# Optimization experiments

Measured on AMD Instinct MI355X. Metric: run time of the kernel, lower is better.

## Reference

```python
import jax, jax.numpy as jnp
import numpy as np

B, S, D, H, M, V, R = 2, 1024, 768, 8, 3072, 32000, 2
HD = D // H  # head_dim = qkv_dim // num_heads


def ln(x, scale, bias, eps=1e-6):
    m = jnp.mean(x, axis=-1, keepdims=True)
    v = jnp.mean(jnp.square(x - m), axis=-1, keepdims=True)
    return (x - m) * jax.lax.rsqrt(v + eps) * scale + bias


def setup_inputs() -> dict:
    key = jax.random.key(0)
    ks = jax.random.split(key, 16)
    r = lambda i, shp, s=0.02: jax.random.normal(ks[i], shp, jnp.float32) * s
    z = lambda shp: jnp.zeros(shp, jnp.float32)
    o = lambda shp: jnp.ones(shp, jnp.float32)
    return {
        'l2r_embed': jax.random.normal(ks[0], (B, S, D), jnp.float32),
        'r2l_embed': jax.random.normal(ks[1], (B, S, D), jnp.float32),
        'temb': jax.random.normal(ks[2], (B, D), jnp.float32),
        'ln_l2r_s': o((D,)), 'ln_l2r_b': z((D,)),
        'ln_r2l_s': o((D,)), 'ln_r2l_b': z((D,)),
        'Wq': r(3, (D, H, HD)), 'bq': z((H, HD)),
        'Wk': r(4, (D, H, HD)), 'bk': z((H, HD)),
        'Wv': r(5, (D, H, HD)), 'bv': z((H, HD)),
        'Wo': r(6, (H, HD, D)), 'bo': z((D,)),
        'ff_ln_s': o((D,)), 'ff_ln_b': z((D,)),
        'ff_w1': r(7, (D, M)), 'ff_b1': z((M,)),
        'ff_w2': r(8, (M, D)), 'ff_b2': z((D,)),
        'tm_w1': r(9, (D, M)), 'tm_b1': z((M,)),
        'tm_w2': r(10, (M, 4 * D)), 'tm_b2': z((4 * D,)),
        'film_w': r(11, (R, 4 * D, 2 * D)), 'film_b': z((R, 2 * D)),
        'r_w1': r(12, (R, D, M)), 'r_b1': z((R, M)),
        'r_w2': r(13, (R, M, D)), 'r_b2': z((R, D)),
        'r_ln_s': o((R, D)), 'r_ln_b': z((R, D)),
        'out_w': r(14, (D, V)), 'out_b': z((V,)),
    }


def reference(l2r_embed, r2l_embed, temb, ln_l2r_s, ln_l2r_b, ln_r2l_s, ln_r2l_b,
              Wq, bq, Wk, bk, Wv, bv, Wo, bo, ff_ln_s, ff_ln_b,
              ff_w1, ff_b1, ff_w2, ff_b2, tm_w1, tm_b1, tm_w2, tm_b2,
              film_w, film_b, r_w1, r_b1, r_w2, r_b2, r_ln_s, r_ln_b,
              out_w, out_b):
    inputs = l2r_embed + r2l_embed
    # prenorm on each direction (temb stays raw)
    l2r_n = ln(l2r_embed, ln_l2r_s, ln_l2r_b)
    r2l_n = ln(r2l_embed, ln_r2l_s, ln_r2l_b)
    # cross attention: query from sum, keys/vals from [temb, l2r, r2l]
    q = jnp.einsum('bsd,dhk->bshk', l2r_n + r2l_n, Wq) + bq
    all_e = jnp.concatenate([temb[:, None, :], l2r_n, r2l_n], axis=1)  # [B, 2S+1, D]
    k = jnp.einsum('bsd,dhk->bshk', all_e, Wk) + bk
    v = jnp.einsum('bsd,dhk->bshk', all_e, Wv) + bv
    q = q / jnp.sqrt(jnp.float32(HD))
    logits = jnp.einsum('bqhd,bkhd->bhqk', q, k)  # [B, H, S, 2S+1]
    idx = jnp.arange(S)
    l2r_mask = idx[:, None] >= idx[None, :]
    r2l_mask = idx[:, None] <= idx[None, :]
    joint = jnp.concatenate(
        [jnp.ones((S, 1), bool), l2r_mask, r2l_mask], axis=-1)[None, None]
    aw = jax.nn.softmax(
        jnp.where(joint, logits, jnp.finfo(jnp.float32).min), axis=-1)
    x = jnp.einsum('bhqk,bkhd->bqhd', aw, v)
    x = jnp.einsum('bqhd,hde->bqe', x, Wo) + bo
    x = x + inputs
    # prenorm FF block
    z = ln(x, ff_ln_s, ff_ln_b)
    z = jax.nn.relu(z @ ff_w1 + ff_b1) @ ff_w2 + ff_b2
    x = x + z
    # residual readout with FiLM conditioning
    t = jax.nn.gelu(temb @ tm_w1 + tm_b1) @ tm_w2 + tm_b2  # [B, 4D]
    for i in range(R):
        film = t @ film_w[i] + film_b[i]  # [B, 2D]
        z = jax.nn.gelu(x @ r_w1[i] + r_b1[i]) @ r_w2[i] + r_b2[i]
        x = ln(x + z, r_ln_s[i], r_ln_b[i])
        a, b = jnp.split(film[:, None, :], 2, axis=-1)
        x = a * x + b
    return x @ out_w + out_b  # [B, S, V]
```

## Files before the change

### kernel.cpp

```cpp
#include <hip/hip_runtime.h>
#include <cstdint>
#include <cstddef>

#define Bb 2
#define Ss 1024
#define Dd 768
#define Hh 8
#define HDh 96
#define Mm 3072
#define Vv 32000
#define KVr 2049

typedef __attribute__((ext_vector_type(8))) short short8v;
typedef __attribute__((ext_vector_type(4))) short short4v;
typedef __attribute__((ext_vector_type(4))) float f32x4;

#define GL16(gp, lp) __builtin_amdgcn_global_load_lds( \
    (const __attribute__((address_space(1))) void*)(gp), \
    (__attribute__((address_space(3))) void*)(lp), 16, 0, 0)

static __device__ __forceinline__ short f2bf(float f) {
  union { float f; unsigned u; } x; x.f = f;
  unsigned r = (x.u + 0x7FFFu + ((x.u >> 16) & 1u)) >> 16;
  return (short)(r & 0xFFFFu);
}

static __device__ __forceinline__ float gelu_f(float v) {
  float u = 0.7978845608028654f * (v + 0.044715f * v * v * v);
  float au = fabsf(u);
  float e = __expf(2.f * au);
  float t = 1.f - 2.f / (e + 1.f);
  return 0.5f * v * (1.f + copysignf(t, u));
}

static __device__ __forceinline__ float blk_sum(float val, float* sh) {
  #pragma unroll
  for (int off = 32; off >= 1; off >>= 1) val += __shfl_xor(val, off);
  __syncthreads();
  if ((threadIdx.x & 63) == 0) sh[threadIdx.x >> 6] = val;
  __syncthreads();
  return sh[0] + sh[1] + sh[2] + sh[3];
}

__global__ __launch_bounds__(256) void prep_kernel(
    const float* __restrict__ l2r, const float* __restrict__ r2l,
    const float* __restrict__ temb,
    const float* __restrict__ s1, const float* __restrict__ b1,
    const float* __restrict__ s2, const float* __restrict__ b2,
    float* __restrict__ inputs, short* __restrict__ qin, short* __restrict__ all_e)
{
  __shared__ float sh[4];
  const int tid = threadIdx.x;
  if (blockIdx.x >= 2048) {
    int b = blockIdx.x - 2048;
    #pragma unroll
    for (int i = 0; i < 3; ++i)
      all_e[(size_t)b * KVr * Dd + tid + i * 256] = f2bf(temb[(size_t)b * Dd + tid + i * 256]);
    return;
  }
  const int row = blockIdx.x;
  const int b = row >> 10, s = row & 1023;
  const float* ap = l2r + (size_t)row * Dd;
  const float* cp = r2l + (size_t)row * Dd;
  float a0 = ap[tid], a1 = ap[tid + 256], a2 = ap[tid + 512];
  float c0 = cp[tid], c1 = cp[tid + 256], c2 = cp[tid + 512];
  float ma = blk_sum(a0 + a1 + a2, sh) * (1.f / 768.f);
  float mc = blk_sum(c0 + c1 + c2, sh) * (1.f / 768.f);
  float va = blk_sum((a0-ma)*(a0-ma) + (a1-ma)*(a1-ma) + (a2-ma)*(a2-ma), sh) * (1.f / 768.f);
  float vc = blk_sum((c0-mc)*(c0-mc) + (c1-mc)*(c1-mc) + (c2-mc)*(c2-mc), sh) * (1.f / 768.f);
  float ia = rsqrtf(va + 1e-6f), ic = rsqrtf(vc + 1e-6f);
  size_t ro = (size_t)row * Dd;
  size_t e1 = ((size_t)b * KVr + 1 + s) * Dd;
  size_t e2 = ((size_t)b * KVr + 1 + Ss + s) * Dd;
  float av[3] = {a0, a1, a2}, cv[3] = {c0, c1, c2};
  #pragma unroll
  for (int i = 0; i < 3; ++i) {
    int c = tid + i * 256;
    float an = (av[i] - ma) * ia * s1[c] + b1[c];
    float cn = (cv[i] - mc) * ic * s2[c] + b2[c];
    inputs[ro + c] = av[i] + cv[i];
    qin[ro + c]    = f2bf(an + cn);
    all_e[e1 + c]  = f2bf(an);
    all_e[e2 + c]  = f2bf(cn);
  }
}

__global__ __launch_bounds__(256) void ln_kernel(
    const float* __restrict__ x, const float* __restrict__ sc, const float* __restrict__ bi,
    short* __restrict__ yb)
{
  __shared__ float sh[4];
  const int row = blockIdx.x, tid = threadIdx.x;
  const float* xr = x + (size_t)row * Dd;
  float v0 = xr[tid], v1 = xr[tid + 256], v2 = xr[tid + 512];
  float m = blk_sum(v0 + v1 + v2, sh) * (1.f / 768.f);
  float var = blk_sum((v0-m)*(v0-m) + (v1-m)*(v1-m) + (v2-m)*(v2-m), sh) * (1.f / 768.f);
  float inv = rsqrtf(var + 1e-6f);
  float vv[3] = {v0, v1, v2};
  #pragma unroll
  for (int i = 0; i < 3; ++i) {
    int c = tid + i * 256;
    yb[(size_t)row * Dd + c] = f2bf((vv[i] - m) * inv * sc[c] + bi[c]);
  }
}

__global__ __launch_bounds__(256) void ln_comb(
    const float* __restrict__ pk,
    const float* __restrict__ bias, const float* __restrict__ res,
    const float* __restrict__ sc, const float* __restrict__ bi,
    const float* __restrict__ film, float* __restrict__ yf, short* __restrict__ yb)
{
  __shared__ float sh[4];
  const int row = blockIdx.x, tid = threadIdx.x;
  const size_t PS = (size_t)2048 * 768;
  size_t ro = (size_t)row * Dd;
  float vv[3];
  #pragma unroll
  for (int i = 0; i < 3; ++i) {
    int c = tid + i * 256;
    float v = bias[c] + res[ro + c];
    #pragma unroll
    for (int s = 0; s < 4; ++s) v += pk[s * PS + ro + c];
    vv[i] = v;
  }
  float m = blk_sum(vv[0] + vv[1] + vv[2], sh) * (1.f / 768.f);
  float var = blk_sum((vv[0]-m)*(vv[0]-m) + (vv[1]-m)*(vv[1]-m) + (vv[2]-m)*(vv[2]-m), sh) * (1.f / 768.f);
  float inv = rsqrtf(var + 1e-6f);
  int bb = row >> 10;
  #pragma unroll
  for (int i = 0; i < 3; ++i) {
    int c = tid + i * 256;
    float o = (vv[i] - m) * inv * sc[c] + bi[c];
    o = film[(size_t)bb * 1536 + c] * o + film[(size_t)bb * 1536 + 768 + c];
    if (yf) yf[ro + c] = o;
    if (yb) yb[ro + c] = f2bf(o);
  }
}

__global__ __launch_bounds__(256) void combine_kernel(
    const float* __restrict__ pk,
    const float* __restrict__ bias, const float* __restrict__ res,
    float* __restrict__ yf, short* __restrict__ yb)
{
  const int row = blockIdx.x, tid = threadIdx.x;
  const size_t PS = (size_t)2048 * 768;
  size_t ro = (size_t)row * Dd;
  #pragma unroll
  for (int i = 0; i < 3; ++i) {
    int c = tid + i * 256;
    float v = bias[c] + res[ro + c];
    #pragma unroll
    for (int s = 0; s < 4; ++s) v += pk[s * PS + ro + c];
    yf[ro + c] = v;
    yb[ro + c] = f2bf(v);
  }
}

__global__ __launch_bounds__(256) void convT(const float* __restrict__ W, short* __restrict__ Wt,
                                             int K, int N, int ntile)
{
  __shared__ short T[64][72];
  const int bn = blockIdx.x % ntile, bk = blockIdx.x / ntile;
  const int k0 = bk * 64, n0 = bn * 64, tid = threadIdx.x;
  #pragma unroll
  for (int i = 0; i < 4; ++i) {
    int id = i * 256 + tid;
    int r = id >> 4, c4 = (id & 15) * 4;
    float4 w4 = *(const float4*)(W + (size_t)(k0 + r) * N + n0 + c4);
    T[c4 + 0][r] = f2bf(w4.x);
    T[c4 + 1][r] = f2bf(w4.y);
    T[c4 + 2][r] = f2bf(w4.z);
    T[c4 + 3][r] = f2bf(w4.w);
  }
  __syncthreads();
  #pragma unroll
  for (int i = 0; i < 4; ++i) {
    int id = i * 256 + tid;
    int n = id >> 4, k4 = (id & 15) * 4;
    short4v s = *(const short4v*)&T[n][k4];
    *(short4v*)(Wt + (size_t)(n0 + n) * K + k0 + k4) = s;
  }
}

__global__ __launch_bounds__(256) void convT4(const float* __restrict__ W0, const float* __restrict__ W1,
                                              const float* __restrict__ W2, const float* __restrict__ W3,
                                              const float* __restrict__ bk, const float* __restrict__ bv,
                                              short* __restrict__ Wt, float* __restrict__ kvb)
{
  __shared__ short T[64][72];
  const int tid = threadIdx.x;
  if (blockIdx.x == 576) {
    #pragma unroll
    for (int i = 0; i < 6; ++i) {
      int c = i * 256 + tid;
      if (c < 1536) kvb[c] = (c < 768) ? bk[c] : bv[c - 768];
    }
    return;
  }
  const int wsel = blockIdx.x / 144, rem = blockIdx.x % 144;
  const float* W = wsel == 0 ? W0 : wsel == 1 ? W1 : wsel == 2 ? W2 : W3;
  short* dst = Wt + (size_t)wsel * 768 * 768;
  const int bn = rem % 12, bk2 = rem / 12;
  const int k0 = bk2 * 64, n0 = bn * 64;
  #pragma unroll
  for (int i = 0; i < 4; ++i) {
    int id = i * 256 + tid;
    int r = id >> 4, c4 = (id & 15) * 4;
    float4 w4 = *(const float4*)(W + (size_t)(k0 + r) * 768 + n0 + c4);
    T[c4 + 0][r] = f2bf(w4.x);
    T[c4 + 1][r] = f2bf(w4.y);
    T[c4 + 2][r] = f2bf(w4.z);
    T[c4 + 3][r] = f2bf(w4.w);
  }
  __syncthreads();
  #pragma unroll
  for (int i = 0; i < 4; ++i) {
    int id = i * 256 + tid;
    int n = id >> 4, k4 = (id & 15) * 4;
    short4v s = *(const short4v*)&T[n][k4];
    *(short4v*)(dst + (size_t)(n0 + n) * 768 + k0 + k4) = s;
  }
}

template<int ACT>
__global__ __launch_bounds__(256, 4) void gemm_bf(
    const short* __restrict__ A, const short* __restrict__ Bt,
    const float* __restrict__ bias, const float* __restrict__ res,
    float* __restrict__ C, short* __restrict__ Cbf, float* __restrict__ Cpart,
    int M, int N, int K, float scale, int mtiles, int ntiles, int ksplit)
{
  __shared__ short As[2][4096];
  __shared__ short Bs[2][4096];
  const int tid = threadIdx.x, lane = tid & 63, wv = tid >> 6;
  const int l15 = lane & 15, l4 = lane >> 4;

  const int nwg = gridDim.x;
  const int qc = nwg >> 3, rc = nwg & 7;
  const int xcd = blockIdx.x & 7, idx = blockIdx.x >> 3;
  const int wgid = (xcd < rc ? xcd * (qc + 1) : rc * (qc + 1) + (xcd - rc) * qc) + idx;
  const int by = wgid % mtiles;
  const int rest = wgid / mtiles;
  const int bx = rest % ntiles;
  const int sp = rest / ntiles;
  const int kper = K / ksplit;
  const int kbeg = sp * kper;
  const int NT = kper >> 5;

  const int m0 = by * 128, n0 = bx * 128;
  const int wm = (wv >> 1) * 64, wn = (wv & 1) * 64;

  const int srow = lane >> 2, schunk = lane & 3;
  const int scsw = (schunk ^ ((srow >> 1) & 3)) << 3;
  const short* sA = A + (size_t)(m0 + wv * 32 + srow) * K + kbeg + scsw;
  const short* sB = Bt + (size_t)(n0 + wv * 32 + srow) * K + kbeg + scsw;
  const int stBase = wv * 1024;
  const int frsw = (l4 ^ ((l15 >> 1) & 3)) << 3;

  f32x4 acc[4][4];
  const f32x4 zz = {0.f, 0.f, 0.f, 0.f};
  #pragma unroll
  for (int i = 0; i < 4; ++i)
    #pragma unroll
    for (int j = 0; j < 4; ++j) acc[i][j] = zz;

  GL16(sA, &As[0][stBase]);
  GL16(sA + (size_t)16 * K, &As[0][stBase + 512]);
  GL16(sB, &Bs[0][stBase]);
  GL16(sB + (size_t)16 * K, &Bs[0][stBase + 512]);

  int buf = 0;
  for (int t = 0; t < NT; ++t) {
    if (t + 1 < NT) {
      int k0 = (t + 1) << 5;
      GL16(sA + k0, &As[buf ^ 1][stBase]);
      GL16(sA + (size_t)16 * K + k0, &As[buf ^ 1][stBase + 512]);
      GL16(sB + k0, &Bs[buf ^ 1][stBase]);
      GL16(sB + (size_t)16 * K + k0, &Bs[buf ^ 1][stBase + 512]);
      asm volatile("s_waitcnt vmcnt(4)" ::: "memory");
    } else {
      asm volatile("s_waitcnt vmcnt(0)" ::: "memory");
    }
    __builtin_amdgcn_s_barrier();

    short8v af[4], bfv[4];
    #pragma unroll
    for (int mi = 0; mi < 4; ++mi)
      af[mi] = *(const short8v*)&As[buf][(wm + mi * 16 + l15) * 32 + frsw];
    #pragma unroll
    for (int ni = 0; ni < 4; ++ni)
      bfv[ni] = *(const short8v*)&Bs[buf][(wn + ni * 16 + l15) * 32 + frsw];
    __builtin_amdgcn_s_setprio(1);
    #pragma unroll
    for (int mi = 0; mi < 4; ++mi)
      #pragma unroll
      for (int ni = 0; ni < 4; ++ni)
        acc[mi][ni] = __builtin_amdgcn_mfma_f32_16x16x32_bf16(af[mi], bfv[ni], acc[mi][ni], 0, 0, 0);
    __builtin_amdgcn_s_setprio(0);
    if (t + 1 < NT) __builtin_amdgcn_s_barrier();
    buf ^= 1;
  }

  if (Cpart) {
    float* Cp = Cpart + (size_t)sp * M * N;
    #pragma unroll
    for (int mi = 0; mi < 4; ++mi)
      #pragma unroll
      for (int r = 0; r < 4; ++r) {
        int row = m0 + wm + mi * 16 + l4 * 4 + r;
        if (row >= M) continue;
        size_t rb = (size_t)row * N;
        #pragma unroll
        for (int ni = 0; ni < 4; ++ni)
          Cp[rb + n0 + wn + ni * 16 + l15] = acc[mi][ni][r];
      }
    return;
  }

  #pragma unroll
  for (int mi = 0; mi < 4; ++mi) {
    #pragma unroll
    for (int r = 0; r < 4; ++r) {
      int row = m0 + wm + mi * 16 + l4 * 4 + r;
      if (row >= M) continue;
      size_t rb = (size_t)row * N;
      #pragma unroll
      for (int ni = 0; ni < 4; ++ni) {
        int col = n0 + wn + ni * 16 + l15;
        float val = (acc[mi][ni][r] + bias[col]) * scale;
        if (ACT == 1) val = fmaxf(val, 0.f);
        if (ACT == 2) val = gelu_f(val);
        if (res) val += res[rb + col];
        if (C)   C[rb + col] = val;
        if (Cbf) Cbf[rb + col] = f2bf(val);
      }
    }
  }
}

__global__ __launch_bounds__(512, 2) void gemm256(
    const short* __restrict__ A, const short* __restrict__ Bt,
    const float* __restrict__ bias, float* __restrict__ C,
    int M, int N, int K, int mtiles)
{
  __shared__ short As[2][16384];
  __shared__ short Bs[2][16384];
  const int tid = threadIdx.x, lane = tid & 63, wv = tid >> 6;
  const int l15 = lane & 15, l4 = lane >> 4;

  const int nwg = gridDim.x;
  const int qc = nwg >> 3, rc = nwg & 7;
  const int xcd = blockIdx.x & 7, idx = blockIdx.x >> 3;
  const int wgid = (xcd < rc ? xcd * (qc + 1) : rc * (qc + 1) + (xcd - rc) * qc) + idx;
  const int by = wgid % mtiles, bx = wgid / mtiles;
  const int m0 = by * 256, n0 = bx * 256;
  const int wm = (wv >> 2) * 128, wn = (wv & 3) * 64;

  const int srow = lane >> 2, schunk = lane & 3;
  const int scsw = (schunk ^ ((srow >> 1) & 3)) << 3;
  const short* sA = A + (size_t)(m0 + wv * 16 + srow) * K + scsw;
  const short* sB = Bt + (size_t)(n0 + wv * 16 + srow) * K + scsw;
  const int stBase = wv * 512;
  const int frsw = (l4 ^ ((l15 >> 1) & 3)) << 3;

  #define STG_A(b, kk, ko) do { \
    GL16(sA + (ko) + (kk) * 32,                  &As[b][(kk) * 8192 + stBase]); \
    GL16(sA + (size_t)128 * K + (ko) + (kk) * 32, &As[b][(kk) * 8192 + 4096 + stBase]); } while (0)
  #define STG_B(b, kk, ko) do { \
    GL16(sB + (ko) + (kk) * 32,                  &Bs[b][(kk) * 8192 + stBase]); \
    GL16(sB + (size_t)128 * K + (ko) + (kk) * 32, &Bs[b][(kk) * 8192 + 4096 + stBase]); } while (0)
  #define ARD(b, kk, row) (*(const short8v*)&As[b][(kk) * 8192 + (row) * 32 + frsw])
  #define BRD(b, kk, row) (*(const short8v*)&Bs[b][(kk) * 8192 + (row) * 32 + frsw])

  f32x4 acc[8][4];
  const f32x4 zz = {0.f, 0.f, 0.f, 0.f};
  #pragma unroll
  for (int i = 0; i < 8; ++i)
    #pragma unroll
    for (int j = 0; j < 4; ++j) acc[i][j] = zz;

  const int NT = K >> 6;

  STG_A(0, 0, 0); STG_B(0, 0, 0); STG_A(0, 1, 0); STG_B(0, 1, 0);
  asm volatile("s_waitcnt vmcnt(4)" ::: "memory");
  __builtin_amdgcn_s_barrier();

  int buf = 0;
  for (int t = 0; t < NT; ++t) {
    const bool pf = (t + 1 < NT);
    const int k1 = (t + 1) << 6;
    short8v af[4], bfv[4];

    #pragma unroll
    for (int mi = 0; mi < 4; ++mi) af[mi] = ARD(buf, 0, wm + mi * 16 + l15);
    #pragma unroll
    for (int ni = 0; ni < 4; ++ni) bfv[ni] = BRD(buf, 0, wn + ni * 16 + l15);
    if (pf) STG_A(buf ^ 1, 0, k1);
    __builtin_amdgcn_s_barrier();
    asm volatile("s_waitcnt lgkmcnt(0)" ::: "memory");
    __builtin_amdgcn_sched_barrier(0);
    __builtin_amdgcn_s_setprio(1);
    #pragma unroll
    for (int mi = 0; mi < 4; ++mi)
      #pragma unroll
      for (int ni = 0; ni < 4; ++ni)
        acc[mi][ni] = __builtin_amdgcn_mfma_f32_16x16x32_bf16(af[mi], bfv[ni], acc[mi][ni], 0, 0, 0);
    __builtin_amdgcn_s_setprio(0);
    __builtin_amdgcn_s_barrier();

    #pragma unroll
    for (int mi = 0; mi < 4; ++mi) af[mi] = ARD(buf, 0, wm + 64 + mi * 16 + l15);
    if (pf) STG_B(buf ^ 1, 0, k1);
    __builtin_amdgcn_s_barrier();
    asm volatile("s_waitcnt lgkmcnt(0)" ::: "memory");
    __builtin_amdgcn_sched_barrier(0);
    __builtin_amdgcn_s_setprio(1);
    #pragma unroll
    for (int mi = 0; mi < 4; ++mi)
      #pragma unroll
      for (int ni = 0; ni < 4; ++ni)
        acc[4 + mi][ni] = __builtin_amdgcn_mfma_f32_16x16x32_bf16(af[mi], bfv[ni], acc[4 + mi][ni], 0, 0, 0);
    __builtin_amdgcn_s_setprio(0);
    if (pf) asm volatile("s_waitcnt vmcnt(4)" ::: "memory");
    else    asm volatile("s_waitcnt vmcnt(0)" ::: "memory");
    __builtin_amdgcn_s_barrier();

    #pragma unroll
    for (int mi = 0; mi < 4; ++mi) af[mi] = ARD(buf, 1, wm + mi * 16 + l15);
    #pragma unroll
    for (int ni = 0; ni < 4; ++ni) bfv[ni] = BRD(buf, 1, wn + ni * 16 + l15);
    if (pf) STG_A(buf ^ 1, 1, k1);
    __builtin_amdgcn_s_barrier();
    asm volatile("s_waitcnt lgkmcnt(0)" ::: "memory");
    __builtin_amdgcn_sched_barrier(0);
    __builtin_amdgcn_s_setprio(1);
    #pragma unroll
    for (int mi = 0; mi < 4; ++mi)
      #pragma unroll
      for (int ni = 0; ni < 4; ++ni)
        acc[mi][ni] = __builtin_amdgcn_mfma_f32_16x16x32_bf16(af[mi], bfv[ni], acc[mi][ni], 0, 0, 0);
    __builtin_amdgcn_s_setprio(0);
    __builtin_amdgcn_s_barrier();

    #pragma unroll
    for (int mi = 0; mi < 4; ++mi) af[mi] = ARD(buf, 1, wm + 64 + mi * 16 + l15);
    if (pf) STG_B(buf ^ 1, 1, k1);
    __builtin_amdgcn_s_barrier();
    asm volatile("s_waitcnt lgkmcnt(0)" ::: "memory");
    __builtin_amdgcn_sched_barrier(0);
    __builtin_amdgcn_s_setprio(1);
    #pragma unroll
    for (int mi = 0; mi < 4; ++mi)
      #pragma unroll
      for (int ni = 0; ni < 4; ++ni)
        acc[4 + mi][ni] = __builtin_amdgcn_mfma_f32_16x16x32_bf16(af[mi], bfv[ni], acc[4 + mi][ni], 0, 0, 0);
    __builtin_amdgcn_s_setprio(0);
    if (pf) asm volatile("s_waitcnt vmcnt(4)" ::: "memory");
    __builtin_amdgcn_s_barrier();

    buf ^= 1;
  }

  #pragma unroll
  for (int mi = 0; mi < 8; ++mi) {
    #pragma unroll
    for (int r = 0; r < 4; ++r) {
      int row = m0 + wm + mi * 16 + l4 * 4 + r;
      size_t rb = (size_t)row * N;
      #pragma unroll
      for (int ni = 0; ni < 4; ++ni) {
        int col = n0 + wn + ni * 16 + l15;
        C[rb + col] = acc[mi][ni][r] + bias[col];
      }
    }
  }
  #undef STG_A
  #undef STG_B
  #undef ARD
  #undef BRD
}

__global__ __launch_bounds__(256) void attn_kernel(
    const short* __restrict__ q, const short* __restrict__ kv, short* __restrict__ o)
{
  __shared__ short Kls[64][104];
  __shared__ short Vt[96][72];
  __shared__ short Pls[4][16][72];

  const int tid = threadIdx.x, lane = tid & 63, w = tid >> 6;
  const int l15 = lane & 15, l4 = lane >> 4;
  const int qt = blockIdx.x & 15;
  const int bh = blockIdx.x >> 4;
  const int h = bh & 7, b = bh >> 3;
  const int qb = qt * 64;
  const int qw = qb + w * 16;

  short8v qf[3];
  {
    const short* qp = q + ((size_t)(b * Ss + qw + l15)) * Dd + h * HDh + l4 * 8;
    #pragma unroll
    for (int kk = 0; kk < 3; ++kk) qf[kk] = *(const short8v*)(qp + kk * 32);
  }

  const f32x4 zz = {0.f, 0.f, 0.f, 0.f};
  f32x4 Oa[6];
  #pragma unroll
  for (int fn = 0; fn < 6; ++fn) Oa[fn] = zz;
  float mrow[4], lrow[4];
  #pragma unroll
  for (int r = 0; r < 4; ++r) { mrow[r] = -3.0e38f; lrow[r] = 0.f; }

  const size_t kvbase = (size_t)b * KVr;

  for (int t = 0; t < 33; ++t) {
    int k0 = t * 64;
    bool l2r_vis = (k0 <= Ss) && (k0 - 1 <= qb + 63);
    int rmaxk = (k0 + 63 > 2 * Ss) ? 2 * Ss : (k0 + 63);
    bool r2l_vis = (k0 + 63 >= Ss + 1) && (rmaxk - (Ss + 1) >= qb);
    if (!(t == 0 || l2r_vis || r2l_vis)) continue;

    __syncthreads();
    #pragma unroll
    for (int i = 0; i < 3; ++i) {
      int id = i * 256 + tid;
      int row = id / 12, cc = (id % 12) * 8;
      const short* kp = kv + (kvbase + k0 + row) * 1536 + h * HDh + cc;
      short8v k8 = *(const short8v*)kp;
      *(short8v*)&Kls[row][cc] = k8;
      short8v v8 = *(const short8v*)(kp + 768);
      #pragma unroll
      for (int j = 0; j < 8; ++j) Vt[cc + j][row] = v8[j];
    }
    __syncthreads();

    f32x4 sc[4];
    #pragma unroll
    for (int nt = 0; nt < 4; ++nt) {
      f32x4 d = zz;
      #pragma unroll
      for (int kk = 0; kk < 3; ++kk) {
        short8v kf = *(const short8v*)&Kls[nt * 16 + l15][kk * 32 + l4 * 8];
        d = __builtin_amdgcn_mfma_f32_16x16x32_bf16(qf[kk], kf, d, 0, 0, 0);
      }
      sc[nt] = d;
    }
    float tmax[4] = {-3.0e38f, -3.0e38f, -3.0e38f, -3.0e38f};
    #pragma unroll
    for (int nt = 0; nt < 4; ++nt)
      #pragma unroll
      for (int r = 0; r < 4; ++r) {
        int qg = qw + l4 * 4 + r;
        int j = k0 + nt * 16 + l15;
        bool vis = (j == 0) ||
                   (j >= 1 && j <= Ss && (j - 1) <= qg) ||
                   (j >= Ss + 1 && j <= 2 * Ss && (j - (Ss + 1)) >= qg);
        if (!vis) sc[nt][r] = -3.0e38f;
        tmax[r] = fmaxf(tmax[r], sc[nt][r]);
      }
    #pragma unroll
    for (int r = 0; r < 4; ++r) {
      #pragma unroll
      for (int off = 8; off >= 1; off >>= 1) tmax[r] = fmaxf(tmax[r], __shfl_xor(tmax[r], off));
    }
    float scl[4];
    #pragma unroll
    for (int r = 0; r < 4; ++r) {
      float mnew = fmaxf(mrow[r], tmax[r]);
      scl[r] = __expf(mrow[r] - mnew);
      mrow[r] = mnew;
    }
    #pragma unroll
    for (int fn = 0; fn < 6; ++fn)
      #pragma unroll
      for (int r = 0; r < 4; ++r) Oa[fn][r] *= scl[r];
    float lad[4] = {0.f, 0.f, 0.f, 0.f};
    #pragma unroll
    for (int nt = 0; nt < 4; ++nt)
      #pragma unroll
      for (int r = 0; r < 4; ++r) {
        float p = __expf(sc[nt][r] - mrow[r]);
        lad[r] += p;
        Pls[w][l4 * 4 + r][nt * 16 + l15] = f2bf(p);
      }
    #pragma unroll
    for (int r = 0; r < 4; ++r) {
      #pragma unroll
      for (int off = 8; off >= 1; off >>= 1) lad[r] += __shfl_xor(lad[r], off);
      lrow[r] = lrow[r] * scl[r] + lad[r];
    }
    __syncthreads();

    short8v pf[2];
    #pragma unroll
    for (int kk = 0; kk < 2; ++kk) pf[kk] = *(const short8v*)&Pls[w][l15][kk * 32 + l4 * 8];
    #pragma unroll
    for (int fn = 0; fn < 6; ++fn) {
      #pragma unroll
      for (int kk = 0; kk < 2; ++kk) {
        short8v vf = *(const short8v*)&Vt[fn * 16 + l15][kk * 32 + l4 * 8];
        Oa[fn] = __builtin_amdgcn_mfma_f32_16x16x32_bf16(pf[kk], vf, Oa[fn], 0, 0, 0);
      }
    }
  }

  #pragma unroll
  for (int fn = 0; fn < 6; ++fn)
    #pragma unroll
    for (int r = 0; r < 4; ++r) {
      int row = qw + l4 * 4 + r;
      int col = h * HDh + fn * 16 + l15;
      o[((size_t)(b * Ss + row)) * Dd + col] = f2bf(Oa[fn][r] / lrow[r]);
    }
}

__global__ __launch_bounds__(256) void thin1(const float* __restrict__ A, const float* __restrict__ W,
                                             float* __restrict__ part, int K, int N, int nblk, int splits)
{
  __shared__ float a0s[64], a1s[64];
  const int nb = blockIdx.x % nblk, ks = blockIdx.x / nblk;
  const int kl = K / splits, kbeg = ks * kl;
  const int tid = threadIdx.x;
  for (int k = tid; k < kl; k += 256) { a0s[k] = A[kbeg + k]; a1s[k] = A[K + kbeg + k]; }
  __syncthreads();
  const int n = nb * 256 + tid;
  float acc0 = 0.f, acc1 = 0.f;
  for (int k = 0; k < kl; ++k) {
    float w = W[(size_t)(kbeg + k) * N + n];
    acc0 = fmaf(a0s[k], w, acc0);
    acc1 = fmaf(a1s[k], w, acc1);
  }
  part[(size_t)ks * 2 * N + n] = acc0;
  part[(size_t)ks * 2 * N + N + n] = acc1;
}

template<int ACT>
__global__ __launch_bounds__(256) void thin2(const float* __restrict__ part,
                                             const float* __restrict__ bias,
                                             float* __restrict__ C, int N, int splits)
{
  const int n = blockIdx.x * 256 + threadIdx.x;
  float a0 = bias[n], a1 = a0;
  for (int s = 0; s < splits; ++s) {
    a0 += part[(size_t)s * 2 * N + n];
    a1 += part[(size_t)s * 2 * N + N + n];
  }
  if (ACT == 2) { a0 = gelu_f(a0); a1 = gelu_f(a1); }
  C[n] = a0; C[N + n] = a1;
}

__global__ __launch_bounds__(256) void film1(const float* __restrict__ A,
                                             const float* __restrict__ W,
                                             float* __restrict__ part)
{
  __shared__ float a0s[48], a1s[48];
  const int nb = blockIdx.x % 12, ks = blockIdx.x / 12;
  const int kbeg = ks * 48, tid = threadIdx.x;
  for (int k = tid; k < 48; k += 256) { a0s[k] = A[kbeg + k]; a1s[k] = A[3072 + kbeg + k]; }
  __syncthreads();
  const int n = nb * 256 + tid;
  const int col = (n >= 1536) ? (n - 1536) : n;
  const float* Wp = W + ((n < 1536) ? (size_t)0 : (size_t)3072 * 1536)
                      + (size_t)kbeg * 1536 + col;
  float acc0 = 0.f, acc1 = 0.f;
  for (int k = 0; k < 48; ++k) {
    float w = Wp[(size_t)k * 1536];
    acc0 = fmaf(a0s[k], w, acc0);
    acc1 = fmaf(a1s[k], w, acc1);
  }
  part[(size_t)ks * 6144 + n] = acc0;
  part[(size_t)ks * 6144 + 3072 + n] = acc1;
}

__global__ __launch_bounds__(256) void film2(const float* __restrict__ part,
                                             const float* __restrict__ fb,
                                             float* __restrict__ f0, float* __restrict__ f1)
{
  const int n = blockIdx.x * 256 + threadIdx.x;
  float a0 = fb[n], a1 = a0;
  for (int s = 0; s < 64; ++s) {
    a0 += part[(size_t)s * 6144 + n];
    a1 += part[(size_t)s * 6144 + 3072 + n];
  }
  float* dst = (n < 1536) ? f0 : f1;
  const int c = (n >= 1536) ? (n - 1536) : n;
  dst[c] = a0;
  dst[1536 + c] = a1;
}

static void gemm_launch(int act, const short* A, const short* Bt, const float* bias,
                        const float* res, float* C, short* Cbf, float* Cpart,
                        int M, int N, int K, float scale, int ksplit, hipStream_t s)
{
  int mt = (M + 127) >> 7, nt = N >> 7;
  dim3 grid(mt * nt * ksplit), blk(256);
  if (act == 1)      gemm_bf<1><<<grid, blk, 0, s>>>(A, Bt, bias, res, C, Cbf, Cpart, M, N, K, scale, mt, nt, ksplit);
  else if (act == 2) gemm_bf<2><<<grid, blk, 0, s>>>(A, Bt, bias, res, C, Cbf, Cpart, M, N, K, scale, mt, nt, ksplit);
  else               gemm_bf<0><<<grid, blk, 0, s>>>(A, Bt, bias, res, C, Cbf, Cpart, M, N, K, scale, mt, nt, ksplit);
}

static void conv_launch(const float* W, short* Wt, int K, int N, hipStream_t s)
{
  int nt = N >> 6, kt = K >> 6;
  convT<<<dim3(nt * kt), dim3(256), 0, s>>>(W, Wt, K, N, nt);
}

static void thin_launch(int act, const float* A, const float* W, const float* bias,
                        float* C, float* part, int K, int N, hipStream_t s)
{
  int nblk = N >> 8, splits = 64;
  thin1<<<dim3(nblk * splits), dim3(256), 0, s>>>(A, W, part, K, N, nblk, splits);
  if (act == 2) thin2<2><<<dim3(nblk), dim3(256), 0, s>>>(part, bias, C, N, splits);
  else          thin2<0><<<dim3(nblk), dim3(256), 0, s>>>(part, bias, C, N, splits);
}

extern "C" void kernel_launch(void* const* d_in, const int* in_sizes, int n_in,
                              void* d_out, int out_size, void* d_ws, size_t ws_size,
                              hipStream_t stream)
{
  (void)in_sizes; (void)n_in; (void)out_size; (void)ws_size;
  const float* l2r      = (const float*)d_in[0];
  const float* r2l      = (const float*)d_in[1];
  const float* temb     = (const float*)d_in[2];
  const float* ln_l2r_s = (const float*)d_in[3];
  const float* ln_l2r_b = (const float*)d_in[4];
  const float* ln_r2l_s = (const float*)d_in[5];
  const float* ln_r2l_b = (const float*)d_in[6];
  const float* Wq = (const float*)d_in[7];
  const float* bq = (const float*)d_in[8];
  const float* Wk = (const float*)d_in[9];
  const float* bk = (const float*)d_in[10];
  const float* Wv = (const float*)d_in[11];
  const float* bv = (const float*)d_in[12];
  const float* Wo = (const float*)d_in[13];
  const float* bo = (const float*)d_in[14];
  const float* ff_ln_s = (const float*)d_in[15];
  const float* ff_ln_b = (const float*)d_in[16];
  const float* ff_w1 = (const float*)d_in[17];
  const float* ff_b1 = (const float*)d_in[18];
  const float* ff_w2 = (const float*)d_in[19];
  const float* ff_b2 = (const float*)d_in[20];
  const float* tm_w1 = (const float*)d_in[21];
  const float* tm_b1 = (const float*)d_in[22];
  const float* tm_w2 = (const float*)d_in[23];
  const float* tm_b2 = (const float*)d_in[24];
  const float* film_w = (const float*)d_in[25];
  const float* film_b = (const float*)d_in[26];
  const float* r_w1 = (const float*)d_in[27];
  const float* r_b1 = (const float*)d_in[28];
  const float* r_w2 = (const float*)d_in[29];
  const float* r_b2 = (const float*)d_in[30];
  const float* r_ln_s = (const float*)d_in[31];
  const float* r_ln_b = (const float*)d_in[32];
  const float* out_w = (const float*)d_in[33];
  const float* out_b = (const float*)d_in[34];

  uint8_t* base = (uint8_t*)d_ws;
  short* qin_bf  = (short*)(base + 0);
  short* alle_bf = (short*)(base + 3145728);
  short* qb      = (short*)(base + 9440256);
  short* kvbuf   = (short*)(base + 12585984);
  short* attn_bf = (short*)(base + 25175040);
  float* inputs  = (float*)(base + 28320768);
  float* xbuf    = (float*)(base + 34612224);
  short* xn_bf   = (short*)(base + 40903680);
  short* big_bf  = (short*)(base + 44049408);
  float* x2f     = (float*)(base + 56632320);
  short* x2bf    = (short*)(base + 62923776);
  float* x3f     = (float*)(base + 72360960);
  short* x3bf    = (short*)(base + 78652416);
  short* x4bf    = (short*)(base + 81798144);
  short* wslot   = (short*)(base + 84943872);
  uint8_t* sm    = base + 89662464;
  float* t1    = (float*)sm;
  float* tb    = (float*)(sm + 24576);
  float* f0    = (float*)(sm + 49152);
  float* f1    = (float*)(sm + 61440);
  float* kvbia = (float*)(sm + 73728);
  float* part2 = (float*)(base + 44049408);
  float* partK = (float*)(base + 0);
  short* outwT = (short*)(base + 0);

  const float qscale = 0.1020620726159658f;
  dim3 blk(256);

  thin_launch(2, temb, tm_w1, tm_b1, t1, part2, 768, 3072, stream);
  thin_launch(0, t1, tm_w2, tm_b2, tb, part2, 3072, 3072, stream);
  film1<<<dim3(12 * 64), blk, 0, stream>>>(tb, film_w, part2);
  film2<<<dim3(12), blk, 0, stream>>>(part2, film_b, f0, f1);

  prep_kernel<<<2050, blk, 0, stream>>>(l2r, r2l, temb, ln_l2r_s, ln_l2r_b, ln_r2l_s, ln_r2l_b,
                                        inputs, qin_bf, alle_bf);

  convT4<<<dim3(577), blk, 0, stream>>>(Wq, Wk, Wv, Wo, bk, bv, wslot, kvbia);

  gemm_launch(0, qin_bf, wslot, bq, nullptr, nullptr, qb, nullptr, 2048, 768, 768, qscale, 1, stream);
  gemm_launch(0, alle_bf, wslot + (size_t)768 * 768, kvbia, nullptr, nullptr, kvbuf, nullptr, 4098, 1536, 768, 1.f, 1, stream);

  attn_kernel<<<256, blk, 0, stream>>>(qb, kvbuf, attn_bf);

  gemm_launch(0, attn_bf, wslot + (size_t)3 * 768 * 768, bo, inputs, xbuf, nullptr, nullptr, 2048, 768, 768, 1.f, 1, stream);
  ln_kernel<<<2048, blk, 0, stream>>>(xbuf, ff_ln_s, ff_ln_b, xn_bf);

  conv_launch(ff_w1, wslot, 768, 3072, stream);
  gemm_launch(1, xn_bf, wslot, ff_b1, nullptr, nullptr, big_bf, nullptr, 2048, 3072, 768, 1.f, 1, stream);
  conv_launch(ff_w2, wslot, 3072, 768, stream);
  gemm_launch(0, big_bf, wslot, nullptr, nullptr, nullptr, nullptr, partK, 2048, 768, 3072, 1.f, 4, stream);
  combine_kernel<<<2048, blk, 0, stream>>>(partK, ff_b2, xbuf, x2f, x2bf);

  conv_launch(r_w1, wslot, 768, 3072, stream);
  gemm_launch(2, x2bf, wslot, r_b1, nullptr, nullptr, big_bf, nullptr, 2048, 3072, 768, 1.f, 1, stream);
  conv_launch(r_w2, wslot, 3072, 768, stream);
  gemm_launch(0, big_bf, wslot, nullptr, nullptr, nullptr, nullptr, partK, 2048, 768, 3072, 1.f, 4, stream);
  ln_comb<<<2048, blk, 0, stream>>>(partK, r_b2, x2f, r_ln_s, r_ln_b, f0, x3f, x3bf);

  conv_launch(r_w1 + (size_t)768 * 3072, wslot, 768, 3072, stream);
  gemm_launch(2, x3bf, wslot, r_b1 + 3072, nullptr, nullptr, big_bf, nullptr, 2048, 3072, 768, 1.f, 1, stream);
  conv_launch(r_w2 + (size_t)3072 * 768, wslot, 3072, 768, stream);
  gemm_launch(0, big_bf, wslot, nullptr, nullptr, nullptr, nullptr, partK, 2048, 768, 3072, 1.f, 4, stream);
  ln_comb<<<2048, blk, 0, stream>>>(partK, r_b2 + 768, x3f, r_ln_s + 768, r_ln_b + 768, f1, nullptr, x4bf);

  conv_launch(out_w, outwT, 768, 32000, stream);
  gemm256<<<dim3(8 * 125), dim3(512), 0, stream>>>(x4bf, outwT, out_b, (float*)d_out,
                                                   2048, 32000, 768, 8);
}
```

Baseline: 645.3 us.

## Shrink gemm256 K-step and fuse split-K reductions into time-MLP chain kernels

The 256x256 GEMM kernel now stages 32-wide K slices per iteration instead of 64, halving LDS usage and using one barrier-separated load/compute phase per step with fewer intra-iteration barriers. Separately, the temb MLP chain no longer launches thin2 reduction kernels. The next split-K stage sums the partials, adds bias and applies gelu while loading its input. This cuts kernel launches in the small serial prologue, but each block now redundantly re-reduces 64 partials, and the GEMM runs twice as many iterations with less prefetch depth.

```diff
diff --git a/kernel.cpp b/kernel.cpp
--- a/kernel.cpp
+++ b/kernel.cpp
@@ -342,8 +342,8 @@
     const float* __restrict__ bias, float* __restrict__ C,
     int M, int N, int K, int mtiles)
 {
-  __shared__ short As[2][16384];
-  __shared__ short Bs[2][16384];
+  __shared__ short As[2][8192];
+  __shared__ short Bs[2][8192];
   const int tid = threadIdx.x, lane = tid & 63, wv = tid >> 6;
   const int l15 = lane & 15, l4 = lane >> 4;
 
@@ -357,19 +357,10 @@
 
   const int srow = lane >> 2, schunk = lane & 3;
   const int scsw = (schunk ^ ((srow >> 1) & 3)) << 3;
-  const short* sA = A + (size_t)(m0 + wv * 16 + srow) * K + scsw;
-  const short* sB = Bt + (size_t)(n0 + wv * 16 + srow) * K + scsw;
-  const int stBase = wv * 512;
+  const short* sA = A + (size_t)(m0 + wv * 32 + srow) * K + scsw;
+  const short* sB = Bt + (size_t)(n0 + wv * 32 + srow) * K + scsw;
+  const int ldsoff = wv * 1024;
   const int frsw = (l4 ^ ((l15 >> 1) & 3)) << 3;
-
-  #define STG_A(b, kk, ko) do { \
-    GL16(sA + (ko) + (kk) * 32,                  &As[b][(kk) * 8192 + stBase]); \
-    GL16(sA + (size_t)128 * K + (ko) + (kk) * 32, &As[b][(kk) * 8192 + 4096 + stBase]); } while (0)
-  #define STG_B(b, kk, ko) do { \
-    GL16(sB + (ko) + (kk) * 32,                  &Bs[b][(kk) * 8192 + stBase]); \
-    GL16(sB + (size_t)128 * K + (ko) + (kk) * 32, &Bs[b][(kk) * 8192 + 4096 + stBase]); } while (0)
-  #define ARD(b, kk, row) (*(const short8v*)&As[b][(kk) * 8192 + (row) * 32 + frsw])
-  #define BRD(b, kk, row) (*(const short8v*)&Bs[b][(kk) * 8192 + (row) * 32 + frsw])
 
   f32x4 acc[8][4];
   const f32x4 zz = {0.f, 0.f, 0.f, 0.f};
@@ -378,24 +369,34 @@
     #pragma unroll
     for (int j = 0; j < 4; ++j) acc[i][j] = zz;
 
-  const int NT = K >> 6;
-
-  STG_A(0, 0, 0); STG_B(0, 0, 0); STG_A(0, 1, 0); STG_B(0, 1, 0);
-  asm volatile("s_waitcnt vmcnt(4)" ::: "memory");
-  __builtin_amdgcn_s_barrier();
-
-  int buf = 0;
+  const int NT = K >> 5;
+
+  GL16(sA, &As[0][ldsoff]);
+  GL16(sA + (size_t)16 * K, &As[0][ldsoff + 512]);
+  GL16(sB, &Bs[0][ldsoff]);
+  GL16(sB + (size_t)16 * K, &Bs[0][ldsoff + 512]);
+
   for (int t = 0; t < NT; ++t) {
-    const bool pf = (t + 1 < NT);
-    const int k1 = (t + 1) << 6;
+    const int buf = t & 1;
+    if (t + 1 < NT) {
+      const int k0 = (t + 1) << 5;
+      GL16(sA + k0, &As[buf ^ 1][ldsoff]);
+      GL16(sA + (size_t)16 * K + k0, &As[buf ^ 1][ldsoff + 512]);
+      GL16(sB + k0, &Bs[buf ^ 1][ldsoff]);
+      GL16(sB + (size_t)16 * K + k0, &Bs[buf ^ 1][ldsoff + 512]);
+      asm volatile("s_waitcnt vmcnt(4)" ::: "memory");
+    } else {
+      asm volatile("s_waitcnt vmcnt(0)" ::: "memory");
+    }
+    __builtin_amdgcn_s_barrier();
+
     short8v af[4], bfv[4];
-
-    #pragma unroll
-    for (int mi = 0; mi < 4; ++mi) af[mi] = ARD(buf, 0, wm + mi * 16 + l15);
-    #pragma unroll
-    for (int ni = 0; ni < 4; ++ni) bfv[ni] = BRD(buf, 0, wn + ni * 16 + l15);
-    if (pf) STG_A(buf ^ 1, 0, k1);
-    __builtin_amdgcn_s_barrier();
+    #pragma unroll
+    for (int ni = 0; ni < 4; ++ni)
+      bfv[ni] = *(const short8v*)&Bs[buf][(wn + ni * 16 + l15) * 32 + frsw];
+    #pragma unroll
+    for (int mi = 0; mi < 4; ++mi)
+      af[mi] = *(const short8v*)&As[buf][(wm + mi * 16 + l15) * 32 + frsw];
     asm volatile("s_waitcnt lgkmcnt(0)" ::: "memory");
     __builtin_amdgcn_sched_barrier(0);
     __builtin_amdgcn_s_setprio(1);
@@ -405,12 +406,9 @@
       for (int ni = 0; ni < 4; ++ni)
         acc[mi][ni] = __builtin_amdgcn_mfma_f32_16x16x32_bf16(af[mi], bfv[ni], acc[mi][ni], 0, 0, 0);
     __builtin_amdgcn_s_setprio(0);
-    __builtin_amdgcn_s_barrier();
-
-    #pragma unroll
-    for (int mi = 0; mi < 4; ++mi) af[mi] = ARD(buf, 0, wm + 64 + mi * 16 + l15);
-    if (pf) STG_B(buf ^ 1, 0, k1);
-    __builtin_amdgcn_s_barrier();
+    #pragma unroll
+    for (int mi = 0; mi < 4; ++mi)
+      af[mi] = *(const short8v*)&As[buf][(wm + 64 + mi * 16 + l15) * 32 + frsw];
     asm volatile("s_waitcnt lgkmcnt(0)" ::: "memory");
     __builtin_amdgcn_sched_barrier(0);
     __builtin_amdgcn_s_setprio(1);
@@ -420,44 +418,7 @@
       for (int ni = 0; ni < 4; ++ni)
         acc[4 + mi][ni] = __builtin_amdgcn_mfma_f32_16x16x32_bf16(af[mi], bfv[ni], acc[4 + mi][ni], 0, 0, 0);
     __builtin_amdgcn_s_setprio(0);
-    if (pf) asm volatile("s_waitcnt vmcnt(4)" ::: "memory");
-    else    asm volatile("s_waitcnt vmcnt(0)" ::: "memory");
     __builtin_amdgcn_s_barrier();
-
-    #pragma unroll
-    for (int mi = 0; mi < 4; ++mi) af[mi] = ARD(buf, 1, wm + mi * 16 + l15);
-    #pragma unroll
-    for (int ni = 0; ni < 4; ++ni) bfv[ni] = BRD(buf, 1, wn + ni * 16 + l15);
-    if (pf) STG_A(buf ^ 1, 1, k1);
-    __builtin_amdgcn_s_barrier();
-    asm volatile("s_waitcnt lgkmcnt(0)" ::: "memory");
-    __builtin_amdgcn_sched_barrier(0);
-    __builtin_amdgcn_s_setprio(1);
-    #pragma unroll
-    for (int mi = 0; mi < 4; ++mi)
-      #pragma unroll
-      for (int ni = 0; ni < 4; ++ni)
-        acc[mi][ni] = __builtin_amdgcn_mfma_f32_16x16x32_bf16(af[mi], bfv[ni], acc[mi][ni], 0, 0, 0);
-    __builtin_amdgcn_s_setprio(0);
-    __builtin_amdgcn_s_barrier();
-
-    #pragma unroll
-    for (int mi = 0; mi < 4; ++mi) af[mi] = ARD(buf, 1, wm + 64 + mi * 16 + l15);
-    if (pf) STG_B(buf ^ 1, 1, k1);
-    __builtin_amdgcn_s_barrier();
-    asm volatile("s_waitcnt lgkmcnt(0)" ::: "memory");
-    __builtin_amdgcn_sched_barrier(0);
-    __builtin_amdgcn_s_setprio(1);
-    #pragma unroll
-    for (int mi = 0; mi < 4; ++mi)
-      #pragma unroll
-      for (int ni = 0; ni < 4; ++ni)
-        acc[4 + mi][ni] = __builtin_amdgcn_mfma_f32_16x16x32_bf16(af[mi], bfv[ni], acc[4 + mi][ni], 0, 0, 0);
-    __builtin_amdgcn_s_setprio(0);
-    if (pf) asm volatile("s_waitcnt vmcnt(4)" ::: "memory");
-    __builtin_amdgcn_s_barrier();
-
-    buf ^= 1;
   }
 
   #pragma unroll
@@ -473,10 +434,6 @@
       }
     }
   }
-  #undef STG_A
-  #undef STG_B
-  #undef ARD
-  #undef BRD
 }
 
 __global__ __launch_bounds__(256) void attn_kernel(
@@ -632,29 +589,45 @@
   part[(size_t)ks * 2 * N + N + n] = acc1;
 }
 
-template<int ACT>
-__global__ __launch_bounds__(256) void thin2(const float* __restrict__ part,
-                                             const float* __restrict__ bias,
-                                             float* __restrict__ C, int N, int splits)
-{
-  const int n = blockIdx.x * 256 + threadIdx.x;
-  float a0 = bias[n], a1 = a0;
-  for (int s = 0; s < splits; ++s) {
-    a0 += part[(size_t)s * 2 * N + n];
-    a1 += part[(size_t)s * 2 * N + N + n];
-  }
-  if (ACT == 2) { a0 = gelu_f(a0); a1 = gelu_f(a1); }
-  C[n] = a0; C[N + n] = a1;
-}
-
-__global__ __launch_bounds__(256) void film1(const float* __restrict__ A,
-                                             const float* __restrict__ W,
-                                             float* __restrict__ part)
+__global__ __launch_bounds__(256) void thin1p(
+    const float* __restrict__ pin, const float* __restrict__ bin,
+    const float* __restrict__ W, float* __restrict__ part)
 {
   __shared__ float a0s[48], a1s[48];
   const int nb = blockIdx.x % 12, ks = blockIdx.x / 12;
   const int kbeg = ks * 48, tid = threadIdx.x;
-  for (int k = tid; k < 48; k += 256) { a0s[k] = A[kbeg + k]; a1s[k] = A[3072 + kbeg + k]; }
+  for (int j = tid; j < 96; j += 256) {
+    int row = j / 48, k = j % 48;
+    float v = bin[kbeg + k];
+    for (int s = 0; s < 64; ++s) v += pin[(size_t)s * 6144 + (size_t)row * 3072 + kbeg + k];
+    v = gelu_f(v);
+    if (row) a1s[k] = v; else a0s[k] = v;
+  }
+  __syncthreads();
+  const int n = nb * 256 + tid;
+  float acc0 = 0.f, acc1 = 0.f;
+  for (int k = 0; k < 48; ++k) {
+    float w = W[(size_t)(kbeg + k) * 3072 + n];
+    acc0 = fmaf(a0s[k], w, acc0);
+    acc1 = fmaf(a1s[k], w, acc1);
+  }
+  part[(size_t)ks * 6144 + n] = acc0;
+  part[(size_t)ks * 6144 + 3072 + n] = acc1;
+}
+
+__global__ __launch_bounds__(256) void film1p(
+    const float* __restrict__ pin, const float* __restrict__ bin,
+    const float* __restrict__ W, float* __restrict__ part)
+{
+  __shared__ float a0s[48], a1s[48];
+  const int nb = blockIdx.x % 12, ks = blockIdx.x / 12;
+  const int kbeg = ks * 48, tid = threadIdx.x;
+  for (int j = tid; j < 96; j += 256) {
+    int row = j / 48, k = j % 48;
+    float v = bin[kbeg + k];
+    for (int s = 0; s < 64; ++s) v += pin[(size_t)s * 6144 + (size_t)row * 3072 + kbeg + k];
+    if (row) a1s[k] = v; else a0s[k] = v;
+  }
   __syncthreads();
   const int n = nb * 256 + tid;
   const int col = (n >= 1536) ? (n - 1536) : n;
@@ -701,15 +674,6 @@
 {
   int nt = N >> 6, kt = K >> 6;
   convT<<<dim3(nt * kt), dim3(256), 0, s>>>(W, Wt, K, N, nt);
-}
-
-static void thin_launch(int act, const float* A, const float* W, const float* bias,
-                        float* C, float* part, int K, int N, hipStream_t s)
-{
-  int nblk = N >> 8, splits = 64;
-  thin1<<<dim3(nblk * splits), dim3(256), 0, s>>>(A, W, part, K, N, nblk, splits);
-  if (act == 2) thin2<2><<<dim3(nblk), dim3(256), 0, s>>>(part, bias, C, N, splits);
-  else          thin2<0><<<dim3(nblk), dim3(256), 0, s>>>(part, bias, C, N, splits);
 }
 
 extern "C" void kernel_launch(void* const* d_in, const int* in_sizes, int n_in,
@@ -770,22 +734,22 @@
   short* x4bf    = (short*)(base + 81798144);
   short* wslot   = (short*)(base + 84943872);
   uint8_t* sm    = base + 89662464;
-  float* t1    = (float*)sm;
-  float* tb    = (float*)(sm + 24576);
-  float* f0    = (float*)(sm + 49152);
-  float* f1    = (float*)(sm + 61440);
-  float* kvbia = (float*)(sm + 73728);
-  float* part2 = (float*)(base + 44049408);
+  float* f0    = (float*)(sm + 0);
+  float* f1    = (float*)(sm + 12288);
+  float* kvbia = (float*)(sm + 24576);
+  float* part2a = (float*)(base + 44049408);
+  float* part2b = (float*)(base + 44049408 + 1572864);
+  float* part2c = (float*)(base + 44049408 + 3145728);
   float* partK = (float*)(base + 0);
   short* outwT = (short*)(base + 0);
 
   const float qscale = 0.1020620726159658f;
   dim3 blk(256);
 
-  thin_launch(2, temb, tm_w1, tm_b1, t1, part2, 768, 3072, stream);
-  thin_launch(0, t1, tm_w2, tm_b2, tb, part2, 3072, 3072, stream);
-  film1<<<dim3(12 * 64), blk, 0, stream>>>(tb, film_w, part2);
-  film2<<<dim3(12), blk, 0, stream>>>(part2, film_b, f0, f1);
+  thin1<<<dim3(12 * 64), blk, 0, stream>>>(temb, tm_w1, part2a, 768, 3072, 12, 64);
+  thin1p<<<dim3(12 * 64), blk, 0, stream>>>(part2a, tm_b1, tm_w2, part2b);
+  film1p<<<dim3(12 * 64), blk, 0, stream>>>(part2b, tm_b2, film_w, part2c);
+  film2<<<dim3(12), blk, 0, stream>>>(part2c, film_b, f0, f1);
 
   prep_kernel<<<2050, blk, 0, stream>>>(l2r, r2l, temb, ln_l2r_s, ln_l2r_b, ln_r2l_s, ln_r2l_b,
                                         inputs, qin_bf, alle_bf);
```

Result: faster. 626.6 us (-2.9%).
